# Performance work log

Hardware: AMD Instinct MI355X
Metric: run time of the kernel (lower is better)

The kernel has to match this reference:

```python
import jax, jax.numpy as jnp
import numpy as np

N_HEADS = 16


def _apply_rope(x, cos, sin):
    # x: [B, H, S, hd]; cos/sin: [>=S, hd/2]
    S = x.shape[2]
    cos = cos[None, None, :S]
    sin = sin[None, None, :S]
    x1, x2 = x[..., ::2], x[..., 1::2]
    # interleaved rotate, matching torch stack(...).flatten(-2)
    return jnp.stack([x1 * cos - x2 * sin, x1 * sin + x2 * cos], axis=-1).reshape(x.shape)


def setup_inputs() -> dict:
    key = jax.random.key(0)
    B, S, D = 2, 2048, 1024
    hd = D // N_HEADS
    k1, k2, k3 = jax.random.split(key, 3)
    x = jax.random.normal(k1, (B, S, D), dtype=jnp.float32)
    # standard RoPE tables (theta=10000)
    inv_freq = 1.0 / (10000.0 ** (np.arange(0, hd, 2, dtype=np.float32) / hd))  # [hd/2]
    freqs = np.outer(np.arange(S, dtype=np.float32), inv_freq)  # [S, hd/2]
    rope_cos = jnp.asarray(np.cos(freqs), dtype=jnp.float32)
    rope_sin = jnp.asarray(np.sin(freqs), dtype=jnp.float32)
    W_qkv = jax.random.normal(k2, (D, 3 * D), dtype=jnp.float32) * (D ** -0.5)
    W_out = jax.random.normal(k3, (D, D), dtype=jnp.float32) * (D ** -0.5)
    return {"x": x, "rope_cos": rope_cos, "rope_sin": rope_sin, "W_qkv": W_qkv, "W_out": W_out}


def reference(x, rope_cos, rope_sin, W_qkv, W_out):
    B, S, D = x.shape
    H = N_HEADS
    hd = D // H
    qkv = (x @ W_qkv).reshape(B, S, 3, H, hd)  # fused QKV projection
    q = qkv[:, :, 0].transpose(0, 2, 1, 3)  # [B,H,S,hd]
    k = qkv[:, :, 1].transpose(0, 2, 1, 3)
    v = qkv[:, :, 2].transpose(0, 2, 1, 3)
    q = _apply_rope(q, rope_cos, rope_sin)
    k = _apply_rope(k, rope_cos, rope_sin)
    scale = hd ** -0.5
    scores = jnp.einsum('bhqd,bhkd->bhqk', q, k) * scale  # [B,H,S,S]
    causal = jnp.tril(jnp.ones((S, S), dtype=bool))
    scores = jnp.where(causal, scores, jnp.finfo(scores.dtype).min)
    attn = jax.nn.softmax(scores, axis=-1)
    out = jnp.einsum('bhqk,bhkd->bhqd', attn, v)  # [B,H,S,hd]
    out = out.transpose(0, 2, 1, 3).reshape(B, S, D)
    return out @ W_out  # dropout is identity in eval mode
```

## Files before the change

kernel.cpp:

```cpp
#include <hip/hip_runtime.h>
#include <stdint.h>

typedef short bf16x8 __attribute__((ext_vector_type(8)));
typedef short bf16x4 __attribute__((ext_vector_type(4)));
typedef float f32x4 __attribute__((ext_vector_type(4)));

#define HD 64
#define NH 16
#define SEQ 2048
#define BATCH 2
#define DM 1024
#define TOK (BATCH * SEQ)

__device__ __forceinline__ unsigned short f2bf(float f) {
    union { float f; unsigned u; } a; a.f = f;
    unsigned r = a.u + 0x7fffu + ((a.u >> 16) & 1u);
    return (unsigned short)(r >> 16);
}
__device__ __forceinline__ float bf2f(unsigned short u) {
    union { unsigned u; float f; } a; a.u = ((unsigned)u) << 16;
    return a.f;
}

__device__ __forceinline__ float fexp2(float x) {
#if __has_builtin(__builtin_amdgcn_exp2f)
    return __builtin_amdgcn_exp2f(x);
#else
    return exp2f(x);
#endif
}
__device__ __forceinline__ float frcp(float x) {
#if __has_builtin(__builtin_amdgcn_rcpf)
    return __builtin_amdgcn_rcpf(x);
#else
    return 1.0f / x;
#endif
}

__device__ __forceinline__ f32x4 mfma16(bf16x4 a, bf16x4 b, f32x4 c) {
#if defined(__HIP_DEVICE_COMPILE__)
    return __builtin_amdgcn_mfma_f32_16x16x16bf16_1k(a, b, c, 0, 0, 0);
#else
    (void)a; (void)b;
    return c;
#endif
}

__device__ __forceinline__ void gld_lds16(const unsigned short* g, unsigned short* l) {
#if __has_builtin(__builtin_amdgcn_global_load_lds)
    __builtin_amdgcn_global_load_lds(
        (const __attribute__((address_space(1))) unsigned int*)g,
        (__attribute__((address_space(3))) unsigned int*)l, 16, 0, 0);
#else
    *(bf16x8*)l = *(const bf16x8*)g;
#endif
}

__global__ void __launch_bounds__(256) k_prep(const float* __restrict__ x,
                                              unsigned short* __restrict__ xb,
                                              const float* __restrict__ wqkv,
                                              unsigned short* __restrict__ wqkvt,
                                              const float* __restrict__ wout,
                                              unsigned short* __restrict__ woutt) {
    int bid = blockIdx.x;
    int tid = threadIdx.x;
    if (bid < 4096) {
        int i = (bid * 256 + tid) * 4;
        float4 v = *(const float4*)(x + i);
        union { ushort4 v; unsigned short s[4]; } o;
        o.s[0] = f2bf(v.x); o.s[1] = f2bf(v.y); o.s[2] = f2bf(v.z); o.s[3] = f2bf(v.w);
        *(ushort4*)(xb + i) = o.v;
        return;
    }
    const float* W; unsigned short* Wt; int N, t;
    if (bid < 7168) { W = wqkv; Wt = wqkvt; N = 3 * DM; t = bid - 4096; }
    else            { W = wout; Wt = woutt; N = DM;     t = bid - 7168; }
    int ntx = N >> 5;
    int bx = t % ntx, by = t / ntx;
    int tx = tid & 31, ty = tid >> 5;
    __shared__ float tile[32][33];
    for (int r = 0; r < 4; ++r) {
        int k = by * 32 + ty + r * 8;
        int n = bx * 32 + tx;
        tile[ty + r * 8][tx] = W[(size_t)k * N + n];
    }
    __syncthreads();
    for (int r = 0; r < 4; ++r) {
        int n = bx * 32 + ty + r * 8;
        int k = by * 32 + tx;
        Wt[(size_t)n * DM + k] = f2bf(tile[tx][ty + r * 8]);
    }
}

#define BKK 32

template <int MODE>
__device__ __forceinline__ void gemm_core(const unsigned short* __restrict__ A,
                                          const unsigned short* __restrict__ Bt,
                                          int K, int N,
                                          float* __restrict__ C,
                                          unsigned short* __restrict__ qbuf,
                                          unsigned short* __restrict__ kbuf,
                                          unsigned short* __restrict__ vt) {
    __shared__ unsigned short As0[128 * BKK];
    __shared__ unsigned short As1[128 * BKK];
    __shared__ unsigned short Bs0[128 * BKK];
    __shared__ unsigned short Bs1[128 * BKK];
    int tid = threadIdx.x;
    int lane = tid & 63, wave = tid >> 6;
    int row0 = blockIdx.y * 128;
    int col0 = blockIdx.x * 128;
    int wm = (wave >> 1) * 64, wn = (wave & 1) * 64;
    int fr = lane & 15;
    int quad = lane >> 4;

    f32x4 zero4 = {0.f, 0.f, 0.f, 0.f};
    f32x4 acc[4][4];
    for (int i = 0; i < 4; ++i)
        for (int j = 0; j < 4; ++j) acc[i][j] = zero4;

    auto stage = [&](unsigned short* Ad, unsigned short* Bd, int k0) {
        for (int i = 0; i < 2; ++i) {
            int s2 = i * 256 + tid;
            int r = s2 >> 2, kc = s2 & 3;
            int kk = (kc ^ (r & 3)) * 8;
            gld_lds16(A + (size_t)(row0 + r) * K + k0 + kk, Ad + (i * 256 + wave * 64) * 8);
            gld_lds16(Bt + (size_t)(col0 + r) * K + k0 + kk, Bd + (i * 256 + wave * 64) * 8);
        }
    };
    auto compute = [&](const unsigned short* Al, const unsigned short* Bl) {
        bf16x8 af[4], bf[4];
        for (int i = 0; i < 4; ++i) {
            int rr = wm + i * 16 + fr;
            af[i] = *(const bf16x8*)&Al[rr * BKK + ((quad ^ (rr & 3)) * 8)];
        }
        for (int j = 0; j < 4; ++j) {
            int rr = wn + j * 16 + fr;
            bf[j] = *(const bf16x8*)&Bl[rr * BKK + ((quad ^ (rr & 3)) * 8)];
        }
        for (int i = 0; i < 4; ++i)
            for (int j = 0; j < 4; ++j)
                acc[i][j] = __builtin_amdgcn_mfma_f32_16x16x32_bf16(af[i], bf[j], acc[i][j], 0, 0, 0);
    };

    stage(As0, Bs0, 0);
    __syncthreads();
    for (int k0 = 0; k0 < K; k0 += 2 * BKK) {
        if (k0 + BKK < K) stage(As1, Bs1, k0 + BKK);
        compute(As0, Bs0);
        __syncthreads();
        if (k0 + 2 * BKK < K) stage(As0, Bs0, k0 + 2 * BKK);
        compute(As1, Bs1);
        __syncthreads();
    }

    int rq = (lane >> 4) * 4;
    int cq = lane & 15;
    for (int i = 0; i < 4; ++i)
        for (int j = 0; j < 4; ++j)
            for (int reg = 0; reg < 4; ++reg) {
                int row = row0 + wm + i * 16 + rq + reg;
                int col = col0 + wn + j * 16 + cq;
                float v = acc[i][j][reg];
                if (MODE == 0) {
                    C[(size_t)row * N + col] = v;
                } else {
                    int which = col >> 10;
                    int hc = col & 1023;
                    int h = hc >> 6, d = hc & 63;
                    int b = row >> 11, s = row & (SEQ - 1);
                    int bh = b * NH + h;
                    unsigned short bv = f2bf(v);
                    if (which == 0)      qbuf[((size_t)bh * SEQ + s) * HD + d] = bv;
                    else if (which == 1) kbuf[((size_t)bh * SEQ + s) * HD + d] = bv;
                    else                 vt[((size_t)bh * HD + d) * SEQ + s] = bv;
                }
            }
}

__global__ void __launch_bounds__(256) k_gemm_qkv(const unsigned short* __restrict__ A,
                                                  const unsigned short* __restrict__ Bt,
                                                  unsigned short* __restrict__ qbuf,
                                                  unsigned short* __restrict__ kbuf,
                                                  unsigned short* __restrict__ vt) {
    gemm_core<1>(A, Bt, DM, 3 * DM, nullptr, qbuf, kbuf, vt);
}

__global__ void __launch_bounds__(256) k_gemm_out(const unsigned short* __restrict__ A,
                                                  const unsigned short* __restrict__ Bt,
                                                  float* __restrict__ C) {
    gemm_core<0>(A, Bt, DM, DM, C, nullptr, nullptr, nullptr);
}

__global__ void k_rope(unsigned short* __restrict__ qbuf, unsigned short* __restrict__ kbuf,
                       const float* __restrict__ cosb, const float* __restrict__ sinb) {
    int t = blockIdx.x * 256 + threadIdx.x;
    int c = t & 7;
    int row = (t >> 3) & 65535;
    int which = t >> 19;
    unsigned short* p = (which ? kbuf : qbuf) + (size_t)row * HD + c * 8;
    float sc = which ? 1.0f : (0.125f * 1.44269504f);
    int s = row & (SEQ - 1);
    const float* cs = cosb + s * 32 + c * 4;
    const float* sn = sinb + s * 32 + c * 4;
    bf16x8 v = *(const bf16x8*)p;
    bf16x8 o;
    for (int i = 0; i < 4; ++i) {
        float x1 = bf2f((unsigned short)v[2 * i]);
        float x2 = bf2f((unsigned short)v[2 * i + 1]);
        float cc = cs[i], ss = sn[i];
        o[2 * i]     = (short)f2bf((x1 * cc - x2 * ss) * sc);
        o[2 * i + 1] = (short)f2bf((x1 * ss + x2 * cc) * sc);
    }
    *(bf16x8*)p = o;
}

#define VSTR 72

__global__ void __launch_bounds__(256, 4) k_attn(const unsigned short* __restrict__ qbuf,
                                                 const unsigned short* __restrict__ kbuf,
                                                 const unsigned short* __restrict__ vt,
                                                 unsigned short* __restrict__ obuf) {
    __shared__ unsigned short Ks[64 * VSTR];
    __shared__ unsigned short Vs[64 * VSTR];

    int tid = threadIdx.x;
    int lane = tid & 63, wave = tid >> 6;
    int bh = blockIdx.y;
    int b = bh >> 4, h = bh & 15;
    int qt = (int)gridDim.x - 1 - (int)blockIdx.x;
    int qb = qt * 64;
    int fr = lane & 15, quad = lane >> 4;
    int Qmin = qb + wave * 16;

    const unsigned short* Qb = qbuf + (size_t)bh * SEQ * HD;
    const unsigned short* Kb = kbuf + (size_t)bh * SEQ * HD;
    const unsigned short* Vb = vt + (size_t)bh * HD * SEQ;

    int qrow = Qmin + fr;
    bf16x8 qf0 = *(const bf16x8*)(Qb + (size_t)qrow * HD + quad * 8);
    bf16x8 qf1 = *(const bf16x8*)(Qb + (size_t)qrow * HD + 32 + quad * 8);

    f32x4 zero4 = {0.f, 0.f, 0.f, 0.f};
    f32x4 o[4];
    for (int j = 0; j < 4; ++j) o[j] = zero4;
    float l = 0.f;

    for (int kt = 0; kt <= qt; ++kt) {
        int kb = kt * 64;
        __syncthreads();
        for (int a = 0; a < 2; ++a) {
            int idx = a * 256 + tid;
            int r = idx >> 3, c8 = (idx & 7) * 8;
            *(bf16x8*)&Ks[r * VSTR + c8] = *(const bf16x8*)(Kb + (size_t)(kb + r) * HD + c8);
            *(bf16x8*)&Vs[r * VSTR + c8] = *(const bf16x8*)(Vb + (size_t)r * SEQ + kb + c8);
        }
        __syncthreads();

        f32x4 sg[4];
        for (int g = 0; g < 4; ++g) {
            int r = g * 16 + fr;
            bf16x8 ka = *(const bf16x8*)&Ks[r * VSTR + quad * 8];
            bf16x8 kc = *(const bf16x8*)&Ks[r * VSTR + 32 + quad * 8];
            f32x4 z = zero4;
            z = __builtin_amdgcn_mfma_f32_16x16x32_bf16(ka, qf0, z, 0, 0, 0);
            z = __builtin_amdgcn_mfma_f32_16x16x32_bf16(kc, qf1, z, 0, 0, 0);
            sg[g] = z;
        }
        if (kt == qt) {
            int q = Qmin + fr;
            for (int g = 0; g < 4; ++g)
                for (int reg = 0; reg < 4; ++reg)
                    if (kb + g * 16 + quad * 4 + reg > q) sg[g][reg] = -1e30f;
        }
        bf16x4 pf[4];
        for (int g = 0; g < 4; ++g) {
            float ps = 0.f;
            bf16x4 pk;
            for (int reg = 0; reg < 4; ++reg) {
                float p = fexp2(sg[g][reg]);
                ps += p;
                pk[reg] = (short)f2bf(p);
            }
            pf[g] = pk;
            l += ps;
        }
        for (int g = 0; g < 4; ++g)
            for (int db = 0; db < 4; ++db) {
                bf16x4 vf = *(const bf16x4*)&Vs[(db * 16 + fr) * VSTR + g * 16 + quad * 4];
                o[db] = mfma16(pf[g], vf, o[db]);
            }
    }

    l += __shfl_xor(l, 16);
    l += __shfl_xor(l, 32);
    float linv[4];
    for (int reg = 0; reg < 4; ++reg)
        linv[reg] = frcp(__shfl(l, quad * 4 + reg));

    for (int db = 0; db < 4; ++db)
        for (int reg = 0; reg < 4; ++reg) {
            int s = Qmin + quad * 4 + reg;
            int d = db * 16 + fr;
            obuf[((size_t)(b * SEQ + s)) * DM + h * HD + d] = f2bf(o[db][reg] * linv[reg]);
        }
}

extern "C" void kernel_launch(void* const* d_in, const int* in_sizes, int n_in,
                              void* d_out, int out_size, void* d_ws, size_t ws_size,
                              hipStream_t stream) {
    const float* x    = (const float*)d_in[0];
    const float* rc   = (const float*)d_in[1];
    const float* rs   = (const float*)d_in[2];
    const float* wqkv = (const float*)d_in[3];
    const float* wout = (const float*)d_in[4];
    float* out = (float*)d_out;

    char* ws = (char*)d_ws;
    size_t off = 0;
    auto alloc = [&](size_t bytes) {
        char* p = ws + off;
        off += (bytes + 255) & ~(size_t)255;
        return p;
    };
    unsigned short* xb    = (unsigned short*)alloc((size_t)TOK * DM * 2);
    unsigned short* wqkvt = (unsigned short*)alloc((size_t)3 * DM * DM * 2);
    unsigned short* woutt = (unsigned short*)alloc((size_t)DM * DM * 2);
    unsigned short* qbuf  = (unsigned short*)alloc((size_t)BATCH * NH * SEQ * HD * 2);
    unsigned short* kbuf  = (unsigned short*)alloc((size_t)BATCH * NH * SEQ * HD * 2);
    unsigned short* vtb   = (unsigned short*)alloc((size_t)BATCH * NH * SEQ * HD * 2);
    unsigned short* obuf  = (unsigned short*)alloc((size_t)TOK * DM * 2);

    k_prep<<<8192, 256, 0, stream>>>(x, xb, wqkv, wqkvt, wout, woutt);
    k_gemm_qkv<<<dim3(3 * DM / 128, TOK / 128), 256, 0, stream>>>(xb, wqkvt, qbuf, kbuf, vtb);
    k_rope<<<4096, 256, 0, stream>>>(qbuf, kbuf, rc, rs);
    k_attn<<<dim3(SEQ / 64, BATCH * NH), 256, 0, stream>>>(qbuf, kbuf, vtb, obuf);
    k_gemm_out<<<dim3(DM / 128, TOK / 128), 256, 0, stream>>>(obuf, woutt, out);
}
```

Baseline: 210.2 us.

## Double-buffer K/V tiles with direct global-to-LDS loads and XOR swizzle

The attention kernel now uses two LDS buffers for the K and V tiles and prefetches the next tile with direct global-to-LDS loads (gld_lds16) while the current tile is computed. The padded 72-stride layout is replaced by a 64-stride layout with an XOR swizzle to avoid bank conflicts. This removes one barrier per tile and overlaps global memory latency with MFMA work. The cost is doubled LDS use, which may reduce occupancy, and it relies on a gld_lds16 helper defined in the unseen part of the file.

```diff
diff --git a/kernel.cpp b/kernel.cpp
--- a/kernel.cpp
+++ b/kernel.cpp
@@ -215,14 +215,14 @@
     *(bf16x8*)p = o;
 }
 
-#define VSTR 72
-
 __global__ void __launch_bounds__(256, 4) k_attn(const unsigned short* __restrict__ qbuf,
                                                  const unsigned short* __restrict__ kbuf,
                                                  const unsigned short* __restrict__ vt,
                                                  unsigned short* __restrict__ obuf) {
-    __shared__ unsigned short Ks[64 * VSTR];
-    __shared__ unsigned short Vs[64 * VSTR];
+    __shared__ unsigned short Ks0[64 * 64];
+    __shared__ unsigned short Ks1[64 * 64];
+    __shared__ unsigned short Vs0[64 * 64];
+    __shared__ unsigned short Vs1[64 * 64];
 
     int tid = threadIdx.x;
     int lane = tid & 63, wave = tid >> 6;
@@ -246,22 +246,24 @@
     for (int j = 0; j < 4; ++j) o[j] = zero4;
     float l = 0.f;
 
-    for (int kt = 0; kt <= qt; ++kt) {
-        int kb = kt * 64;
-        __syncthreads();
+    auto stage = [&](int kb, unsigned short* Kd, unsigned short* Vd) {
         for (int a = 0; a < 2; ++a) {
             int idx = a * 256 + tid;
-            int r = idx >> 3, c8 = (idx & 7) * 8;
-            *(bf16x8*)&Ks[r * VSTR + c8] = *(const bf16x8*)(Kb + (size_t)(kb + r) * HD + c8);
-            *(bf16x8*)&Vs[r * VSTR + c8] = *(const bf16x8*)(Vb + (size_t)r * SEQ + kb + c8);
-        }
-        __syncthreads();
-
+            int r = idx >> 3;
+            int lg = (idx & 7) ^ (r & 7);
+            gld_lds16(Kb + (size_t)(kb + r) * HD + lg * 8, Kd + (a * 256 + wave * 64) * 8);
+            gld_lds16(Vb + (size_t)r * SEQ + kb + lg * 8, Vd + (a * 256 + wave * 64) * 8);
+        }
+    };
+
+    auto compute = [&](int kt, const unsigned short* Kd, const unsigned short* Vd) {
+        int kb = kt * 64;
+        int sw = fr & 7;
         f32x4 sg[4];
         for (int g = 0; g < 4; ++g) {
             int r = g * 16 + fr;
-            bf16x8 ka = *(const bf16x8*)&Ks[r * VSTR + quad * 8];
-            bf16x8 kc = *(const bf16x8*)&Ks[r * VSTR + 32 + quad * 8];
+            bf16x8 ka = *(const bf16x8*)&Kd[r * 64 + ((quad ^ sw) * 8)];
+            bf16x8 kc = *(const bf16x8*)&Kd[r * 64 + (((quad + 4) ^ sw) * 8)];
             f32x4 z = zero4;
             z = __builtin_amdgcn_mfma_f32_16x16x32_bf16(ka, qf0, z, 0, 0, 0);
             z = __builtin_amdgcn_mfma_f32_16x16x32_bf16(kc, qf1, z, 0, 0, 0);
@@ -287,9 +289,24 @@
         }
         for (int g = 0; g < 4; ++g)
             for (int db = 0; db < 4; ++db) {
-                bf16x4 vf = *(const bf16x4*)&Vs[(db * 16 + fr) * VSTR + g * 16 + quad * 4];
+                int d = db * 16 + fr;
+                int pg = ((2 * g + (quad >> 1)) ^ sw) * 8 + (quad & 1) * 4;
+                bf16x4 vf = *(const bf16x4*)&Vd[d * 64 + pg];
                 o[db] = mfma16(pf[g], vf, o[db]);
             }
+    };
+
+    stage(0, Ks0, Vs0);
+    __syncthreads();
+    for (int kt = 0; kt <= qt; kt += 2) {
+        if (kt + 1 <= qt) stage((kt + 1) * 64, Ks1, Vs1);
+        compute(kt, Ks0, Vs0);
+        __syncthreads();
+        if (kt + 1 <= qt) {
+            if (kt + 2 <= qt) stage((kt + 2) * 64, Ks0, Vs0);
+            compute(kt + 1, Ks1, Vs1);
+            __syncthreads();
+        }
     }
 
     l += __shfl_xor(l, 16);
```

Result: faster. 199.8 us (-4.9%).
